# Kernel optimization log

Measured on AMD Instinct MI355X. Metric: run time of the kernel, lower is better.

## Reference

```python
import jax, jax.numpy as jnp
import numpy as np

B, L, DIN = 2, 4096, 1024
W = 64            # windowsize
G, H = 8, 8       # groups, heads per group
DQ = DV = 64
FF = 1024
NEG = -1e30


def rmsnorm(x, gamma, d):
    # F.normalize(x, dim=-1) * sqrt(d) * gamma
    n = jnp.sqrt(jnp.sum(x * x, axis=-1, keepdims=True))
    return x / jnp.maximum(n, 1e-12) * (d ** 0.5) * gamma


def setup_inputs() -> dict:
    key = jax.random.key(0)
    ks = jax.random.split(key, 8)
    s = 0.02
    return {
        "x": jax.random.normal(ks[0], (B, L, DIN), jnp.float32),
        "norm_gamma": jnp.ones((DIN,), jnp.float32),
        "Wq_w": jax.random.normal(ks[1], (G * H * DQ, DIN), jnp.float32) * s,
        "Wq_b": jnp.zeros((G * H * DQ,), jnp.float32),
        "Wkv_w": jax.random.normal(ks[2], (G * (DQ + DV), DIN), jnp.float32) * s,
        "Wkv_b": jnp.zeros((G * (DQ + DV),), jnp.float32),
        "wz_gamma1": jnp.ones((G * H * DV,), jnp.float32),
        "W1_w": jax.random.normal(ks[3], (2 * FF, G * H * DV), jnp.float32) * s,
        "W1_b": jnp.zeros((2 * FF,), jnp.float32),
        "wz_gamma2": jnp.ones((2 * FF,), jnp.float32),
        "W2_w": jax.random.normal(ks[4], (FF, 2 * FF), jnp.float32) * s,
        "W2_b": jnp.zeros((FF,), jnp.float32),
    }


def reference(x, norm_gamma, Wq_w, Wq_b, Wkv_w, Wkv_b,
              wz_gamma1, W1_w, W1_b, wz_gamma2, W2_w, W2_b):
    w2, w4 = W // 2, W // 4
    S = 2 * L // W  # number of query chunks (L % W == 0 -> drop_last path)

    xn = rmsnorm(x, norm_gamma, DIN)
    q = xn @ Wq_w.T + Wq_b          # [B, L, G*H*DQ]
    kv = xn @ Wkv_w.T + Wkv_b       # [B, L, G*(DQ+DV)]

    # pad_to_multiple(kv, W, mod=W//2): L % W == 0 -> append W//2 zeros
    kv = jnp.pad(kv, ((0, 0), (0, w2), (0, 0)))
    k, v = jnp.split(kv, 2, axis=-1)  # each [B, L+W/2, G*DQ]
    # F.pad W//4 both sides, then overlapping windows of size W, stride W//2
    k = jnp.pad(k, ((0, 0), (w4, w4), (0, 0)))  # [B, L+W, G*DQ]
    v = jnp.pad(v, ((0, 0), (w4, w4), (0, 0)))
    idx = jnp.arange(S)[:, None] * w2 + jnp.arange(W)[None, :]  # [S, W] (drop_last applied)
    kwin = k[:, idx].reshape(B, S, W, G, DQ).transpose(0, 3, 1, 2, 4)  # [B,G,S,W,DQ]
    vwin = v[:, idx].reshape(B, S, W, G, DV).transpose(0, 3, 1, 2, 4)  # [B,G,S,W,DV]

    # 'B (S w) (G H D) -> B G H S w D'
    qh = q.reshape(B, S, w2, G, H, DQ).transpose(0, 3, 4, 1, 2, 5)  # [B,G,H,S,w2,DQ]

    qk = jnp.einsum('bghsqd,bgskd->bghsqk', qh, kwin) * (1.0 / DQ ** 0.5)
    # edge masking: first chunk can't see left pad, last chunk can't see right pad
    maskb = jnp.zeros((S, W), bool).at[0, :w4].set(True).at[S - 1, W - w4:].set(True)
    qk = jnp.where(maskb[None, None, None, :, None, :], NEG, qk)
    attn = jax.nn.softmax(qk, axis=-1)
    o = jnp.einsum('bghsqk,bgskd->bghsqd', attn, vwin)
    o = o.transpose(0, 3, 4, 1, 2, 5).reshape(B, L, G * H * DV)  # 'B G H S w D -> B (S w) (G H D)'

    # Wz: RMSNorm -> Linear -> SiLU -> RMSNorm -> Linear -> SiLU (dropout=0)
    z = rmsnorm(o, wz_gamma1, G * H * DV)
    z = jax.nn.silu(z @ W1_w.T + W1_b)
    z = rmsnorm(z, wz_gamma2, 2 * FF)
    z = jax.nn.silu(z @ W2_w.T + W2_b)
    return z
```

## Files before the change

### kernel.cpp

```cpp
#include <hip/hip_runtime.h>
#include <cstdint>

typedef _Float16 f16;
typedef f16 f16x4 __attribute__((ext_vector_type(4)));
typedef f16 f16x8 __attribute__((ext_vector_type(8)));
typedef float f32x4 __attribute__((ext_vector_type(4)));

#define MFMA16(a, b, c) __builtin_amdgcn_mfma_f32_16x16x32_f16(a, b, c, 0, 0, 0)

static __device__ __forceinline__ void gload16(const void* g, void* l) {
    __builtin_amdgcn_global_load_lds(
        (const __attribute__((address_space(1))) uint32_t*)g,
        (__attribute__((address_space(3))) uint32_t*)l, 16, 0, 0);
}

static __device__ __forceinline__ float blockReduceSum256(float v) {
    __shared__ float red[4];
#pragma unroll
    for (int off = 32; off > 0; off >>= 1) v += __shfl_xor(v, off);
    if ((threadIdx.x & 63) == 0) red[threadIdx.x >> 6] = v;
    __syncthreads();
    return red[0] + red[1] + red[2] + red[3];
}

__global__ __launch_bounds__(256) void k_rmsnorm_x(const float* __restrict__ x,
                                                   const float* __restrict__ gamma,
                                                   f16* __restrict__ out) {
    size_t row = blockIdx.x;
    const float4 v = reinterpret_cast<const float4*>(x + row * 1024)[threadIdx.x];
    float ss = v.x * v.x + v.y * v.y + v.z * v.z + v.w * v.w;
    ss = blockReduceSum256(ss);
    float sc = 32.0f / fmaxf(sqrtf(ss), 1e-12f);
    const float4 g = reinterpret_cast<const float4*>(gamma)[threadIdx.x];
    f16x4 o;
    o[0] = (f16)(v.x * sc * g.x); o[1] = (f16)(v.y * sc * g.y);
    o[2] = (f16)(v.z * sc * g.z); o[3] = (f16)(v.w * sc * g.w);
    *reinterpret_cast<f16x4*>(out + row * 1024 + threadIdx.x * 4) = o;
}

template <int D>
__global__ __launch_bounds__(256) void k_rowss(const f16* __restrict__ in,
                                               float* __restrict__ sc) {
    constexpr int PER = D / 256;
    size_t row = blockIdx.x;
    const f16* ir = in + row * D;
    int c0 = threadIdx.x * PER;
    float ss = 0.f;
#pragma unroll
    for (int i = 0; i < PER; i += 8) {
        f16x8 h = *reinterpret_cast<const f16x8*>(ir + c0 + i);
#pragma unroll
        for (int e = 0; e < 8; ++e) { float f = (float)h[e]; ss += f * f; }
    }
    ss = blockReduceSum256(ss);
    if (threadIdx.x == 0)
        sc[row] = sqrtf((float)D) / fmaxf(sqrtf(ss), 1e-12f);
}

__global__ __launch_bounds__(256) void k_cast(const float* __restrict__ in,
                                              f16* __restrict__ out, int n4) {
    int i = blockIdx.x * 256 + threadIdx.x;
    if (i >= n4) return;
    float4 v = reinterpret_cast<const float4*>(in)[i];
    f16x4 o; o[0] = (f16)v.x; o[1] = (f16)v.y; o[2] = (f16)v.z; o[3] = (f16)v.w;
    *reinterpret_cast<f16x4*>(out + (size_t)i * 4) = o;
}

__global__ __launch_bounds__(256) void k_cast_g(const float* __restrict__ in,
                                                f16* __restrict__ out,
                                                const float* __restrict__ gamma,
                                                int kmask, int n4) {
    int i = blockIdx.x * 256 + threadIdx.x;
    if (i >= n4) return;
    float4 v = reinterpret_cast<const float4*>(in)[i];
    int e0 = (i * 4) & kmask;
    f16x4 o;
    o[0] = (f16)(v.x * gamma[e0]); o[1] = (f16)(v.y * gamma[e0 + 1]);
    o[2] = (f16)(v.z * gamma[e0 + 2]); o[3] = (f16)(v.w * gamma[e0 + 3]);
    *reinterpret_cast<f16x4*>(out + (size_t)i * 4) = o;
}

__global__ __launch_bounds__(256) void k_bias_cat(const float* __restrict__ a,
                                                  const float* __restrict__ b,
                                                  float* __restrict__ o) {
    int i = blockIdx.x * 256 + threadIdx.x;
    o[i] = (i < 4096) ? a[i] : b[i - 4096];
}

template <int BN, int EPI, int MODE>
__global__ __launch_bounds__(512, 2) void k_gemm8p(const f16* __restrict__ A,
                                                   const f16* __restrict__ Bt,
                                                   const float* __restrict__ bias,
                                                   const float* __restrict__ rowsc,
                                                   void* __restrict__ Cout,
                                                   int M, int N, int K) {
    constexpr int BM = 256;
    constexpr int WN = BN / 64, WM = 8 / WN, WR = BM / WM;
    constexpr int MW = WR / 16, MH = MW / 2;
    constexpr int LA = 2, LB = BN / 128;
    constexpr int WSTEADY = 2 * (LA + LB), WTAIL = LA + LB;
    constexpr int AK = BM * 32;
    constexpr int BKE = BN * 32;
    constexpr int SE = 2 * AK + 2 * BKE;

    __shared__ alignas(16) f16 lds[2 * SE];

    const int nb = N / BN, mb = M / BM;
    int bn, bm;
    if (MODE == 0) { bn = blockIdx.x & 7; bm = blockIdx.x >> 3; }
    else           { bn = blockIdx.x % nb; bm = blockIdx.x / nb; }
    (void)mb;

    const int tid = threadIdx.x, w = tid >> 6, l = tid & 63;
    const int wm = w / WN, wn = w % WN;
    const int lrow = l & 15, lq = l >> 4;
    const int g = (lrow >> 1) & 3;

    const f16* Ab = A + (size_t)bm * BM * K;
    const f16* Bb = Bt + (size_t)bn * BN * K;
    const int NT = K >> 6;

    int aoff[MW], boff[4];
#pragma unroll
    for (int m = 0; m < MW; ++m)
        aoff[m] = (wm * WR + m * 16 + lrow) * 32 + 8 * (lq ^ g);
#pragma unroll
    for (int n = 0; n < 4; ++n)
        boff[n] = (wn * 64 + n * 16 + lrow) * 32 + 8 * (lq ^ g);

    auto stageA = [&](int k0, f16* region) {
#pragma unroll
        for (int q = 0; q < LA; ++q) {
            int r = q * 128 + w * 16 + (l >> 2);
            int c = 8 * ((l & 3) ^ ((r >> 1) & 3));
            gload16(Ab + (size_t)r * K + k0 + c, region + q * 4096 + w * 512);
        }
    };
    auto stageB = [&](int k0, f16* region) {
#pragma unroll
        for (int q = 0; q < LB; ++q) {
            int r = q * 128 + w * 16 + (l >> 2);
            int c = 8 * ((l & 3) ^ ((r >> 1) & 3));
            gload16(Bb + (size_t)r * K + k0 + c, region + q * 4096 + w * 512);
        }
    };

    f32x4 acc[MW][4] = {};

    stageA(0, lds);
    stageB(0, lds + 2 * AK);
    stageA(32, lds + AK);
    stageB(32, lds + 2 * AK + BKE);
    stageA(64, lds + SE);
    stageB(64, lds + SE + 2 * AK);

    for (int t = 0; t < NT; ++t) {
        f16* sc_ = lds + (t & 1) * SE;
        f16* sn_ = lds + ((t & 1) ^ 1) * SE;
        f16x8 af[MH], bf[4];

        if (t < NT - 1) asm volatile("s_waitcnt vmcnt(%0)" :: "i"(WSTEADY) : "memory");
        else            asm volatile("s_waitcnt vmcnt(%0)" :: "i"(WTAIL) : "memory");
        __builtin_amdgcn_s_barrier();
        __builtin_amdgcn_sched_barrier(0);
        if (t + 1 < NT) stageA((t + 1) * 64 + 32, sn_ + AK);
#pragma unroll
        for (int n = 0; n < 4; ++n)
            bf[n] = *reinterpret_cast<const f16x8*>(sc_ + 2 * AK + boff[n]);
#pragma unroll
        for (int m = 0; m < MH; ++m)
            af[m] = *reinterpret_cast<const f16x8*>(sc_ + aoff[m]);
        __builtin_amdgcn_s_setprio(1);
#pragma unroll
        for (int m = 0; m < MH; ++m)
#pragma unroll
            for (int n = 0; n < 4; ++n)
                acc[m][n] = MFMA16(af[m], bf[n], acc[m][n]);
        __builtin_amdgcn_s_setprio(0);

        __builtin_amdgcn_s_barrier();
        __builtin_amdgcn_sched_barrier(0);
        if (t + 1 < NT) stageB((t + 1) * 64 + 32, sn_ + 2 * AK + BKE);
#pragma unroll
        for (int m = 0; m < MH; ++m)
            af[m] = *reinterpret_cast<const f16x8*>(sc_ + aoff[MH + m]);
        __builtin_amdgcn_s_setprio(1);
#pragma unroll
        for (int m = 0; m < MH; ++m)
#pragma unroll
            for (int n = 0; n < 4; ++n)
                acc[MH + m][n] = MFMA16(af[m], bf[n], acc[MH + m][n]);
        __builtin_amdgcn_s_setprio(0);

        if (t < NT - 1) asm volatile("s_waitcnt vmcnt(%0)" :: "i"(WSTEADY) : "memory");
        else            asm volatile("s_waitcnt vmcnt(0)" ::: "memory");
        __builtin_amdgcn_s_barrier();
        __builtin_amdgcn_sched_barrier(0);
        if (t + 2 < NT) stageA((t + 2) * 64, sc_);
#pragma unroll
        for (int n = 0; n < 4; ++n)
            bf[n] = *reinterpret_cast<const f16x8*>(sc_ + 2 * AK + BKE + boff[n]);
#pragma unroll
        for (int m = 0; m < MH; ++m)
            af[m] = *reinterpret_cast<const f16x8*>(sc_ + AK + aoff[m]);
        __builtin_amdgcn_s_setprio(1);
#pragma unroll
        for (int m = 0; m < MH; ++m)
#pragma unroll
            for (int n = 0; n < 4; ++n)
                acc[m][n] = MFMA16(af[m], bf[n], acc[m][n]);
        __builtin_amdgcn_s_setprio(0);

        __builtin_amdgcn_s_barrier();
        __builtin_amdgcn_sched_barrier(0);
        if (t + 2 < NT) stageB((t + 2) * 64, sc_ + 2 * AK);
#pragma unroll
        for (int m = 0; m < MH; ++m)
            af[m] = *reinterpret_cast<const f16x8*>(sc_ + AK + aoff[MH + m]);
        __builtin_amdgcn_s_setprio(1);
#pragma unroll
        for (int m = 0; m < MH; ++m)
#pragma unroll
            for (int n = 0; n < 4; ++n)
                acc[MH + m][n] = MFMA16(af[m], bf[n], acc[MH + m][n]);
        __builtin_amdgcn_s_setprio(0);
    }

    const size_t row0 = (size_t)bm * BM + wm * WR;
    const int col0 = bn * BN + wn * 64;
    float bsv[4];
#pragma unroll
    for (int n = 0; n < 4; ++n) bsv[n] = bias[col0 + n * 16 + lrow];
#pragma unroll
    for (int m = 0; m < MW; ++m) {
#pragma unroll
        for (int r = 0; r < 4; ++r) {
            const size_t row = row0 + m * 16 + lq * 4 + r;
            float scl = (EPI >= 1) ? rowsc[row] : 1.0f;
#pragma unroll
            for (int n = 0; n < 4; ++n) {
                float v = acc[m][n][r];
                if (EPI >= 1) v = v * scl;
                v += bsv[n];
                if (EPI >= 1) v = v / (1.f + __expf(-v));
                const size_t idx = row * N + col0 + n * 16 + lrow;
                if (EPI == 2) reinterpret_cast<float*>(Cout)[idx] = v;
                else          reinterpret_cast<f16*>(Cout)[idx] = (f16)v;
            }
        }
    }
}

__global__ __launch_bounds__(256) void k_attn(const f16* __restrict__ qkv,
                                              f16* __restrict__ o) {
    __shared__ alignas(16) f16 Ksm[64 * 64];
    __shared__ alignas(16) f16 Vtsm[64 * 64];
    __shared__ alignas(16) f16 Psm[4][64 * 64];
    const int idx = blockIdx.x;
    const int s = idx & 127;
    const int g = (idx >> 7) & 7;
    const int b = idx >> 10;
    const int tid = threadIdx.x;
    const int w = tid >> 6, l = tid & 63;

    const int baseR = s * 32 - 16;
#pragma unroll
    for (int i = 0; i < 2; ++i) {
        const int j = i * 32 + (tid >> 3);
        const int d0 = (tid & 7) * 8;
        const int R = baseR + j;
        f16x8 kvv = {}, vvv = {};
        if (R >= 0 && R < 4096) {
            const f16* rp = qkv + ((size_t)(b * 4096 + R)) * 5120 + 4096 + g * 64 + d0;
            kvv = *reinterpret_cast<const f16x8*>(rp);
            vvv = *reinterpret_cast<const f16x8*>(rp + 512);
        }
        *reinterpret_cast<f16x8*>(&Ksm[j * 64 + d0]) = kvv;
#pragma unroll
        for (int e = 0; e < 8; ++e) Vtsm[(d0 + e) * 64 + j] = vvv[e];
    }

    const int lrow = l & 15, lk = (l >> 4) * 8;
    f16x8 aq[4][2];
#pragma unroll
    for (int m = 0; m < 4; ++m) {
        const int qr = w * 64 + m * 16 + lrow;
        const int h = qr >> 5, qi = qr & 31;
        const f16* qp = qkv + ((size_t)(b * 4096 + s * 32 + qi)) * 5120 + (g * 8 + h) * 64 + lk;
        aq[m][0] = *reinterpret_cast<const f16x8*>(qp);
        aq[m][1] = *reinterpret_cast<const f16x8*>(qp + 32);
    }
    __syncthreads();

    f32x4 acc[4][4] = {};
#pragma unroll
    for (int kk = 0; kk < 2; ++kk) {
        f16x8 bk[4];
#pragma unroll
        for (int n = 0; n < 4; ++n)
            bk[n] = *reinterpret_cast<const f16x8*>(&Ksm[(n * 16 + lrow) * 64 + kk * 32 + lk]);
#pragma unroll
        for (int m = 0; m < 4; ++m)
#pragma unroll
            for (int n = 0; n < 4; ++n)
                acc[m][n] = MFMA16(aq[m][kk], bk[n], acc[m][n]);
    }

    const int nlo = (s == 0) ? 1 : 0;
    const int nhi = (s == 127) ? 3 : 4;
#pragma unroll
    for (int m = 0; m < 4; ++m) {
#pragma unroll
        for (int r = 0; r < 4; ++r) {
            float xv[4];
#pragma unroll
            for (int n = 0; n < 4; ++n) xv[n] = acc[m][n][r] * 0.125f;
            float mx = -1e30f;
            for (int n = nlo; n < nhi; ++n) mx = fmaxf(mx, xv[n]);
#pragma unroll
            for (int off = 8; off > 0; off >>= 1) mx = fmaxf(mx, __shfl_xor(mx, off));
            float pv[4]; float sum = 0.f;
#pragma unroll
            for (int n = 0; n < 4; ++n) {
                float e = (n >= nlo && n < nhi) ? __expf(xv[n] - mx) : 0.f;
                pv[n] = e; sum += e;
            }
#pragma unroll
            for (int off = 8; off > 0; off >>= 1) sum += __shfl_xor(sum, off);
            const float inv = 1.f / sum;
            const int prow = m * 16 + (l >> 4) * 4 + r;
#pragma unroll
            for (int n = 0; n < 4; ++n)
                Psm[w][prow * 64 + n * 16 + lrow] = (f16)(pv[n] * inv);
        }
    }
    __syncthreads();

    f32x4 oacc[4][4] = {};
#pragma unroll
    for (int kk = 0; kk < 2; ++kk) {
        f16x8 ap[4], bv[4];
#pragma unroll
        for (int m = 0; m < 4; ++m)
            ap[m] = *reinterpret_cast<const f16x8*>(&Psm[w][(m * 16 + lrow) * 64 + kk * 32 + lk]);
#pragma unroll
        for (int n = 0; n < 4; ++n)
            bv[n] = *reinterpret_cast<const f16x8*>(&Vtsm[(n * 16 + lrow) * 64 + kk * 32 + lk]);
#pragma unroll
        for (int m = 0; m < 4; ++m)
#pragma unroll
            for (int n = 0; n < 4; ++n)
                oacc[m][n] = MFMA16(ap[m], bv[n], oacc[m][n]);
    }
    const int lr4 = (l >> 4) * 4;
#pragma unroll
    for (int m = 0; m < 4; ++m) {
#pragma unroll
        for (int r = 0; r < 4; ++r) {
            const int qr = w * 64 + m * 16 + lr4 + r;
            const int h = qr >> 5, qi = qr & 31;
            f16* op = o + ((size_t)(b * 4096 + s * 32 + qi)) * 4096 + (g * 8 + h) * 64;
#pragma unroll
            for (int n = 0; n < 4; ++n) op[n * 16 + lrow] = (f16)oacc[m][n][r];
        }
    }
}

extern "C" void kernel_launch(void* const* d_in, const int* in_sizes, int n_in,
                              void* d_out, int out_size, void* d_ws, size_t ws_size,
                              hipStream_t stream) {
    const float* x     = (const float*)d_in[0];
    const float* ng    = (const float*)d_in[1];
    const float* Wq_w  = (const float*)d_in[2];
    const float* Wq_b  = (const float*)d_in[3];
    const float* Wkv_w = (const float*)d_in[4];
    const float* Wkv_b = (const float*)d_in[5];
    const float* g1    = (const float*)d_in[6];
    const float* W1_w  = (const float*)d_in[7];
    const float* W1_b  = (const float*)d_in[8];
    const float* g2    = (const float*)d_in[9];
    const float* W2_w  = (const float*)d_in[10];
    const float* W2_b  = (const float*)d_in[11];
    float* out = (float*)d_out;

    char* p = (char*)d_ws;
    f16* qkv  = (f16*)(p);
    f16* h1   = (f16*)(p);
    f16* xn   = (f16*)(p + 83886080);
    f16* ob   = (f16*)(p + 83886080);
    f16* w1   = (f16*)(p + 150994944);
    f16* w2   = (f16*)(p + 167772160);
    f16* wqkv = (f16*)(p + 171966464);
    float* cb  = (float*)(p + 182452224);
    float* sc1 = (float*)(p + 182472704);
    float* sc2 = (float*)(p + 182505472);

    k_cast<<<4096, 256, 0, stream>>>(Wq_w, wqkv, 4096 * 1024 / 4);
    k_cast<<<1024, 256, 0, stream>>>(Wkv_w, wqkv + 4096 * 1024, 1024 * 1024 / 4);
    k_cast_g<<<8192, 256, 0, stream>>>(W1_w, w1, g1, 4095, 2048 * 4096 / 4);
    k_cast_g<<<2048, 256, 0, stream>>>(W2_w, w2, g2, 2047, 1024 * 2048 / 4);
    k_bias_cat<<<20, 256, 0, stream>>>(Wq_b, Wkv_b, cb);
    k_rmsnorm_x<<<8192, 256, 0, stream>>>(x, ng, xn);

    k_gemm8p<256, 0, 1><<<640, 512, 0, stream>>>(xn, wqkv, cb, nullptr, qkv, 8192, 5120, 1024);

    k_attn<<<2048, 256, 0, stream>>>(qkv, ob);

    k_rowss<4096><<<8192, 256, 0, stream>>>(ob, sc1);
    k_gemm8p<256, 1, 0><<<256, 512, 0, stream>>>(ob, w1, W1_b, sc1, h1, 8192, 2048, 4096);
    k_rowss<2048><<<8192, 256, 0, stream>>>(h1, sc2);
    k_gemm8p<128, 2, 0><<<256, 512, 0, stream>>>(h1, w2, W2_b, sc2, (void*)out, 8192, 1024, 2048);

    (void)in_sizes; (void)n_in; (void)out_size; (void)ws_size;
}
```

Before: 395.4 us.

## Software-pipeline LDS fragment reads ahead of MFMA blocks in GEMM main loop

Restructures the GEMM inner loop so the LDS reads of the next A/B fragments are issued right after each MFMA block, using double-buffered register fragments (afA/afB, bfA/bfB), instead of reading them just before the MFMAs that consume them. Async global-to-LDS staging is reordered to follow the MFMA issue, and waits and barriers are moved to match, including a prologue read before the loop. The aim is to hide LDS read latency behind matrix-core work. The cost is extra register pressure from the doubled fragments, with launch bounds at 512 threads and 2 blocks, plus more barriers per iteration.

```diff
diff --git a/kernel.cpp b/kernel.cpp
--- a/kernel.cpp
+++ b/kernel.cpp
@@ -98,18 +98,17 @@
     constexpr int WN = BN / 64, WM = 8 / WN, WR = BM / WM;
     constexpr int MW = WR / 16, MH = MW / 2;
     constexpr int LA = 2, LB = BN / 128;
-    constexpr int WSTEADY = 2 * (LA + LB), WTAIL = LA + LB;
+    constexpr int WFULL = 2 * (LA + LB), WHALF = LA + LB;
     constexpr int AK = BM * 32;
     constexpr int BKE = BN * 32;
     constexpr int SE = 2 * AK + 2 * BKE;
 
     __shared__ alignas(16) f16 lds[2 * SE];
 
-    const int nb = N / BN, mb = M / BM;
+    const int nb = N / BN;
     int bn, bm;
     if (MODE == 0) { bn = blockIdx.x & 7; bm = blockIdx.x >> 3; }
     else           { bn = blockIdx.x % nb; bm = blockIdx.x / nb; }
-    (void)mb;
 
     const int tid = threadIdx.x, w = tid >> 6, l = tid & 63;
     const int wm = w / WN, wn = w % WN;
@@ -144,8 +143,19 @@
             gload16(Bb + (size_t)r * K + k0 + c, region + q * 4096 + w * 512);
         }
     };
+    auto rdA = [&](f16x8* d, const f16* base, int h) {
+#pragma unroll
+        for (int m = 0; m < MH; ++m)
+            d[m] = *reinterpret_cast<const f16x8*>(base + aoff[h * MH + m]);
+    };
+    auto rdB = [&](f16x8* d, const f16* base) {
+#pragma unroll
+        for (int n = 0; n < 4; ++n)
+            d[n] = *reinterpret_cast<const f16x8*>(base + boff[n]);
+    };
 
     f32x4 acc[MW][4] = {};
+    f16x8 afA[MH], afB[MH], bfA[4], bfB[4];
 
     stageA(0, lds);
     stageB(0, lds + 2 * AK);
@@ -153,77 +163,73 @@
     stageB(32, lds + 2 * AK + BKE);
     stageA(64, lds + SE);
     stageB(64, lds + SE + 2 * AK);
+    asm volatile("s_waitcnt vmcnt(%0)" :: "i"(WFULL) : "memory");
+    __builtin_amdgcn_s_barrier();
+    rdA(afA, lds, 0);
+    rdB(bfA, lds + 2 * AK);
+    __builtin_amdgcn_sched_barrier(0);
 
     for (int t = 0; t < NT; ++t) {
         f16* sc_ = lds + (t & 1) * SE;
         f16* sn_ = lds + ((t & 1) ^ 1) * SE;
-        f16x8 af[MH], bf[4];
-
-        if (t < NT - 1) asm volatile("s_waitcnt vmcnt(%0)" :: "i"(WSTEADY) : "memory");
-        else            asm volatile("s_waitcnt vmcnt(%0)" :: "i"(WTAIL) : "memory");
+
         __builtin_amdgcn_s_barrier();
+        __builtin_amdgcn_s_setprio(1);
+#pragma unroll
+        for (int m = 0; m < MH; ++m)
+#pragma unroll
+            for (int n = 0; n < 4; ++n)
+                acc[m][n] = MFMA16(afA[m], bfA[n], acc[m][n]);
+        __builtin_amdgcn_s_setprio(0);
+        if (t + 1 < NT) stageA((t + 1) * 64 + 32, sn_ + AK);
+        rdA(afB, sc_, 1);
         __builtin_amdgcn_sched_barrier(0);
-        if (t + 1 < NT) stageA((t + 1) * 64 + 32, sn_ + AK);
-#pragma unroll
-        for (int n = 0; n < 4; ++n)
-            bf[n] = *reinterpret_cast<const f16x8*>(sc_ + 2 * AK + boff[n]);
+
+        __builtin_amdgcn_s_barrier();
+        __builtin_amdgcn_s_setprio(1);
 #pragma unroll
         for (int m = 0; m < MH; ++m)
-            af[m] = *reinterpret_cast<const f16x8*>(sc_ + aoff[m]);
-        __builtin_amdgcn_s_setprio(1);
-#pragma unroll
-        for (int m = 0; m < MH; ++m)
-#pragma unroll
-            for (int n = 0; n < 4; ++n)
-                acc[m][n] = MFMA16(af[m], bf[n], acc[m][n]);
+#pragma unroll
+            for (int n = 0; n < 4; ++n)
+                acc[MH + m][n] = MFMA16(afB[m], bfA[n], acc[MH + m][n]);
         __builtin_amdgcn_s_setprio(0);
-
-        __builtin_amdgcn_s_barrier();
-        __builtin_amdgcn_sched_barrier(0);
         if (t + 1 < NT) stageB((t + 1) * 64 + 32, sn_ + 2 * AK + BKE);
-#pragma unroll
-        for (int m = 0; m < MH; ++m)
-            af[m] = *reinterpret_cast<const f16x8*>(sc_ + aoff[MH + m]);
-        __builtin_amdgcn_s_setprio(1);
-#pragma unroll
-        for (int m = 0; m < MH; ++m)
-#pragma unroll
-            for (int n = 0; n < 4; ++n)
-                acc[MH + m][n] = MFMA16(af[m], bf[n], acc[MH + m][n]);
-        __builtin_amdgcn_s_setprio(0);
-
-        if (t < NT - 1) asm volatile("s_waitcnt vmcnt(%0)" :: "i"(WSTEADY) : "memory");
+        if (t < NT - 1) asm volatile("s_waitcnt vmcnt(%0)" :: "i"(WFULL) : "memory");
         else            asm volatile("s_waitcnt vmcnt(0)" ::: "memory");
         __builtin_amdgcn_s_barrier();
+        rdA(afA, sc_ + AK, 0);
+        rdB(bfB, sc_ + 2 * AK + BKE);
         __builtin_amdgcn_sched_barrier(0);
+
+        __builtin_amdgcn_s_barrier();
+        __builtin_amdgcn_s_setprio(1);
+#pragma unroll
+        for (int m = 0; m < MH; ++m)
+#pragma unroll
+            for (int n = 0; n < 4; ++n)
+                acc[m][n] = MFMA16(afA[m], bfB[n], acc[m][n]);
+        __builtin_amdgcn_s_setprio(0);
         if (t + 2 < NT) stageA((t + 2) * 64, sc_);
-#pragma unroll
-        for (int n = 0; n < 4; ++n)
-            bf[n] = *reinterpret_cast<const f16x8*>(sc_ + 2 * AK + BKE + boff[n]);
+        rdA(afB, sc_ + AK, 1);
+        __builtin_amdgcn_sched_barrier(0);
+
+        __builtin_amdgcn_s_barrier();
+        __builtin_amdgcn_s_setprio(1);
 #pragma unroll
         for (int m = 0; m < MH; ++m)
-            af[m] = *reinterpret_cast<const f16x8*>(sc_ + AK + aoff[m]);
-        __builtin_amdgcn_s_setprio(1);
-#pragma unroll
-        for (int m = 0; m < MH; ++m)
-#pragma unroll
-            for (int n = 0; n < 4; ++n)
-                acc[m][n] = MFMA16(af[m], bf[n], acc[m][n]);
+#pragma unroll
+            for (int n = 0; n < 4; ++n)
+                acc[MH + m][n] = MFMA16(afB[m], bfB[n], acc[MH + m][n]);
         __builtin_amdgcn_s_setprio(0);
-
-        __builtin_amdgcn_s_barrier();
-        __builtin_amdgcn_sched_barrier(0);
         if (t + 2 < NT) stageB((t + 2) * 64, sc_ + 2 * AK);
-#pragma unroll
-        for (int m = 0; m < MH; ++m)
-            af[m] = *reinterpret_cast<const f16x8*>(sc_ + AK + aoff[MH + m]);
-        __builtin_amdgcn_s_setprio(1);
-#pragma unroll
-        for (int m = 0; m < MH; ++m)
-#pragma unroll
-            for (int n = 0; n < 4; ++n)
-                acc[MH + m][n] = MFMA16(af[m], bf[n], acc[MH + m][n]);
-        __builtin_amdgcn_s_setprio(0);
+        if (t + 1 < NT) {
+            if (t < NT - 2) asm volatile("s_waitcnt vmcnt(%0)" :: "i"(WFULL) : "memory");
+            else            asm volatile("s_waitcnt vmcnt(%0)" :: "i"(WHALF) : "memory");
+            __builtin_amdgcn_s_barrier();
+            rdA(afA, sn_, 0);
+            rdB(bfA, sn_ + 2 * AK);
+            __builtin_amdgcn_sched_barrier(0);
+        }
     }
 
     const size_t row0 = (size_t)bm * BM + wm * WR;
```

Result: no change. 394.5 us (-0.2%).
